# Kernel optimization log

Measured on AMD Instinct MI355X. Metric: run time of the kernel, lower is better.

## Reference

```python
import jax, jax.numpy as jnp
import numpy as np

N, T1, T2 = 150000, 30000, 8192
E1, E2 = 400000, 160000
F_IN, F_HID, F_OUT = 512, 256, 20


def setup_inputs() -> dict:
    key = jax.random.key(0)
    ks = jax.random.split(key, 10)
    return {
        "x": jax.random.normal(ks[0], (N, F_IN), dtype=jnp.float32),
        "src1": jax.random.randint(ks[1], (E1,), 0, N, dtype=jnp.int32),
        "dst1": jax.random.randint(ks[2], (E1,), 0, T1, dtype=jnp.int32),
        "src2": jax.random.randint(ks[3], (E2,), 0, T1, dtype=jnp.int32),
        "dst2": jax.random.randint(ks[4], (E2,), 0, T2, dtype=jnp.int32),
        "Wl1": jax.random.normal(ks[5], (F_HID, F_IN), dtype=jnp.float32) * 0.05,
        "bl1": jnp.zeros((F_HID,), dtype=jnp.float32),
        "Wr1": jax.random.normal(ks[6], (F_HID, F_IN), dtype=jnp.float32) * 0.05,
        "Wl2": jax.random.normal(ks[7], (F_OUT, F_HID), dtype=jnp.float32) * 0.05,
        "bl2": jnp.zeros((F_OUT,), dtype=jnp.float32),
        "Wr2": jax.random.normal(ks[8], (F_OUT, F_HID), dtype=jnp.float32) * 0.05,
    }


def _sage_conv(x_src, x_tgt, src, dst, num_tgt, Wl, bl, Wr):
    # PyG SAGEConv (mean aggr, root_weight=True, bias on lin_l):
    # out = lin_l(mean_{j in N(i)} x_src[j]) + lin_r(x_tgt[i])
    msg = x_src[src]                                                  # [E, F]
    agg = jax.ops.segment_sum(msg, dst, num_segments=num_tgt)        # [T, F]
    cnt = jax.ops.segment_sum(jnp.ones((src.shape[0],), x_src.dtype), dst,
                              num_segments=num_tgt)                  # [T]
    mean = agg / jnp.maximum(cnt, 1.0)[:, None]
    return mean @ Wl.T + bl + x_tgt @ Wr.T


def reference(x, src1, dst1, src2, dst2, Wl1, bl1, Wr1, Wl2, bl2, Wr2):
    # Layer 1: [N, F_IN] -> [T1, F_HID], relu (eval mode: no dropout)
    h = _sage_conv(x, x[:T1], src1, dst1, T1, Wl1, bl1, Wr1)
    h = jax.nn.relu(h)
    # Layer 2: [T1, F_HID] -> [T2, F_OUT]
    out = _sage_conv(h, h[:T2], src2, dst2, T2, Wl2, bl2, Wr2)
    return jax.nn.log_softmax(out, axis=-1)
```

## Files before the change

### kernel.cpp

```cpp
#include <hip/hip_runtime.h>
#include <math.h>

constexpr int T1N  = 30000;
constexpr int T2N  = 8192;
constexpr int FIN  = 512;
constexpr int FHID = 256;
constexpr int FOUT = 20;

typedef short bf16x8 __attribute__((ext_vector_type(8)));
typedef float f32x4  __attribute__((ext_vector_type(4)));

__device__ __forceinline__ short f2bf(float f) {
    unsigned u = __float_as_uint(f);
    u += 0x7fff + ((u >> 16) & 1);
    return (short)(u >> 16);
}

__device__ __forceinline__ void gload16(const void* g, void* l) {
    __builtin_amdgcn_global_load_lds(
        (const __attribute__((address_space(1))) void*)g,
        (__attribute__((address_space(3))) void*)l, 16, 0, 0);
}

__global__ void count_kernel(const int* __restrict__ dst, int* __restrict__ cnt, int E) {
    int i = blockIdx.x * blockDim.x + threadIdx.x;
    int stride = gridDim.x * blockDim.x;
    for (; i < E; i += stride) atomicAdd(&cnt[dst[i]], 1);
}

__global__ __launch_bounds__(1024) void scan_kernel(const int* __restrict__ cnt,
        int* __restrict__ rs, int* __restrict__ cur, int T) {
    __shared__ int wsum[16];
    int tid = threadIdx.x;
    int lane = tid & 63, wid = tid >> 6;
    int carry = 0;
    for (int base = 0; base < T; base += 1024) {
        int i = base + tid;
        int v = (i < T) ? cnt[i] : 0;
        int s = v;
        #pragma unroll
        for (int off = 1; off < 64; off <<= 1) {
            int t = __shfl_up(s, off, 64);
            if (lane >= off) s += t;
        }
        if (lane == 63) wsum[wid] = s;
        __syncthreads();
        if (wid == 0) {
            int w = (lane < 16) ? wsum[lane] : 0;
            #pragma unroll
            for (int off = 1; off < 16; off <<= 1) {
                int t = __shfl_up(w, off, 64);
                if (lane >= off) w += t;
            }
            if (lane < 16) wsum[lane] = w;
        }
        __syncthreads();
        int excl = s - v + (wid > 0 ? wsum[wid - 1] : 0) + carry;
        if (i < T) { rs[i] = excl; cur[i] = excl; }
        int total = wsum[15];
        __syncthreads();
        carry += total;
    }
    if (tid == 0) rs[T] = carry;
}

__global__ void scatter_kernel(const int* __restrict__ src, const int* __restrict__ dst,
        int* __restrict__ cur, int* __restrict__ ss, int E) {
    int i = blockIdx.x * blockDim.x + threadIdx.x;
    int stride = gridDim.x * blockDim.x;
    for (; i < E; i += stride) {
        int d = dst[i];
        int pos = atomicAdd(&cur[d], 1);
        ss[pos] = src[i];
    }
}

__global__ void convert_x_kernel(const float* __restrict__ x, short* __restrict__ A) {
    size_t i = ((size_t)blockIdx.x * blockDim.x + threadIdx.x) * 8;
    if (i >= (size_t)T1N * FIN) return;
    int r = (int)(i >> 9);
    int k = (int)(i & 511);
    const float* p = x + (size_t)r * FIN + k;
    float4 v0 = *(const float4*)p;
    float4 v1 = *(const float4*)(p + 4);
    bf16x8 o;
    o[0] = f2bf(v0.x); o[1] = f2bf(v0.y); o[2] = f2bf(v0.z); o[3] = f2bf(v0.w);
    o[4] = f2bf(v1.x); o[5] = f2bf(v1.y); o[6] = f2bf(v1.z); o[7] = f2bf(v1.w);
    *(bf16x8*)(A + (size_t)r * 1024 + 512 + k) = o;
}

__global__ void convert_w_kernel(const float* __restrict__ Wl, const float* __restrict__ Wr,
        short* __restrict__ Wcat) {
    int i = (blockIdx.x * blockDim.x + threadIdx.x) * 8;
    if (i >= FHID * 1024) return;
    int n = i >> 10;
    int k = i & 1023;
    const float* sp = (k < 512) ? (Wl + (size_t)n * FIN + k) : (Wr + (size_t)n * FIN + (k - 512));
    float4 v0 = *(const float4*)sp;
    float4 v1 = *(const float4*)(sp + 4);
    bf16x8 o;
    o[0] = f2bf(v0.x); o[1] = f2bf(v0.y); o[2] = f2bf(v0.z); o[3] = f2bf(v0.w);
    o[4] = f2bf(v1.x); o[5] = f2bf(v1.y); o[6] = f2bf(v1.z); o[7] = f2bf(v1.w);
    *(bf16x8*)(Wcat + (size_t)n * 1024 + k) = o;
}

template <int F, typename OT, int OSTR>
__global__ void aggregate_kernel(const float* __restrict__ feat, const int* __restrict__ ss,
        const int* __restrict__ rs, OT* __restrict__ mean, int T) {
    int gw = (int)((blockIdx.x * (size_t)blockDim.x + threadIdx.x) >> 6);
    int lane = threadIdx.x & 63;
    if (gw >= T) return;
    int j0 = rs[gw], j1 = rs[gw + 1];
    float4 a0 = make_float4(0.f, 0.f, 0.f, 0.f);
    float4 a1 = make_float4(0.f, 0.f, 0.f, 0.f);
    constexpr int PER = F / 64;
    for (int j = j0; j < j1; ++j) {
        int s = ss[j];
        const float* p = feat + (size_t)s * F + lane * PER;
        float4 v0 = *(const float4*)p;
        a0.x += v0.x; a0.y += v0.y; a0.z += v0.z; a0.w += v0.w;
        if (PER == 8) {
            float4 v1 = *(const float4*)(p + 4);
            a1.x += v1.x; a1.y += v1.y; a1.z += v1.z; a1.w += v1.w;
        }
    }
    int d = j1 - j0;
    float inv = 1.0f / (float)(d > 1 ? d : 1);
    if constexpr (sizeof(OT) == 2) {
        bf16x8 o;
        o[0] = f2bf(a0.x * inv); o[1] = f2bf(a0.y * inv);
        o[2] = f2bf(a0.z * inv); o[3] = f2bf(a0.w * inv);
        o[4] = f2bf(a1.x * inv); o[5] = f2bf(a1.y * inv);
        o[6] = f2bf(a1.z * inv); o[7] = f2bf(a1.w * inv);
        *(bf16x8*)(mean + (size_t)gw * OSTR + lane * PER) = o;
    } else {
        float* o = (float*)(mean + (size_t)gw * OSTR + lane * PER);
        *(float4*)o = make_float4(a0.x * inv, a0.y * inv, a0.z * inv, a0.w * inv);
        if (PER == 8)
            *(float4*)(o + 4) = make_float4(a1.x * inv, a1.y * inv, a1.z * inv, a1.w * inv);
    }
}

__global__ __launch_bounds__(256, 2) void gemm1_mfma(
        const short* __restrict__ A, const short* __restrict__ W,
        const float* __restrict__ bias, float* __restrict__ h) {
    __shared__ short As[128 * 32];
    __shared__ short Bs[128 * 32];
    int tid = threadIdx.x;
    int wid = tid >> 6, lane = tid & 63;
    int brow = blockIdx.x * 128, bcol = blockIdx.y * 128;
    int wr = (wid >> 1) * 64, wc = (wid & 1) * 64;

    f32x4 acc[4][4] = {};

    int kgrp = lane >> 4;
    int r16 = lane & 15;

    for (int kt = 0; kt < 1024; kt += 32) {
        #pragma unroll
        for (int c2 = 0; c2 < 2; ++c2) {
            int q = wid + c2 * 4;
            int c = q * 64 + lane;
            int row = c >> 2;
            int sl = (c & 3) ^ (row & 3);
            int gr = brow + row; if (gr > T1N - 1) gr = T1N - 1;
            gload16(A + (size_t)gr * 1024 + kt + sl * 8, (char*)As + q * 1024);
            gload16(W + (size_t)(bcol + row) * 1024 + kt + sl * 8, (char*)Bs + q * 1024);
        }
        __syncthreads();

        bf16x8 af[4], bfr[4];
        #pragma unroll
        for (int m = 0; m < 4; ++m) {
            int row = wr + m * 16 + r16;
            int sl = kgrp ^ (row & 3);
            af[m] = *(const bf16x8*)((const char*)As + row * 64 + sl * 16);
        }
        #pragma unroll
        for (int n = 0; n < 4; ++n) {
            int row = wc + n * 16 + r16;
            int sl = kgrp ^ (row & 3);
            bfr[n] = *(const bf16x8*)((const char*)Bs + row * 64 + sl * 16);
        }
        #pragma unroll
        for (int m = 0; m < 4; ++m)
            #pragma unroll
            for (int n = 0; n < 4; ++n)
                acc[m][n] = __builtin_amdgcn_mfma_f32_16x16x32_bf16(
                        af[m], bfr[n], acc[m][n], 0, 0, 0);
        __syncthreads();
    }

    int g4 = lane >> 4;
    #pragma unroll
    for (int n = 0; n < 4; ++n) {
        int col = bcol + wc + n * 16 + r16;
        float bv = bias[col];
        #pragma unroll
        for (int m = 0; m < 4; ++m) {
            #pragma unroll
            for (int r = 0; r < 4; ++r) {
                int row = brow + wr + m * 16 + g4 * 4 + r;
                if (row < T1N) {
                    float v = acc[m][n][r] + bv;
                    h[(size_t)row * FHID + col] = v > 0.f ? v : 0.f;
                }
            }
        }
    }
}

__global__ __launch_bounds__(256) void gemm2_lsm_kernel(const float* __restrict__ mean2,
        const float* __restrict__ h, const float* __restrict__ Wl,
        const float* __restrict__ Wr, const float* __restrict__ bias,
        float* __restrict__ out) {
    __shared__ float Wls[FOUT * FHID];
    __shared__ float Wrs[FOUT * FHID];
    int tid = threadIdx.x;
    for (int i = tid; i < FOUT * FHID / 4; i += 256) {
        ((float4*)Wls)[i] = ((const float4*)Wl)[i];
        ((float4*)Wrs)[i] = ((const float4*)Wr)[i];
    }
    __syncthreads();

    int row = blockIdx.x * 4 + (tid >> 6);
    int lane = tid & 63;
    if (row >= T2N) return;

    float acc[FOUT];
    #pragma unroll
    for (int o = 0; o < FOUT; ++o) acc[o] = 0.f;

    const float* mrow = mean2 + (size_t)row * FHID;
    const float* hrow = h + (size_t)row * FHID;
    #pragma unroll
    for (int kk = 0; kk < 4; ++kk) {
        int k = lane + kk * 64;
        float m = mrow[k];
        float hr = hrow[k];
        #pragma unroll
        for (int o = 0; o < FOUT; ++o)
            acc[o] = fmaf(m, Wls[o * FHID + k], fmaf(hr, Wrs[o * FHID + k], acc[o]));
    }
    #pragma unroll
    for (int o = 0; o < FOUT; ++o)
        #pragma unroll
        for (int off = 32; off > 0; off >>= 1)
            acc[o] += __shfl_down(acc[o], off, 64);

    if (lane == 0) {
        float mx = -1e30f;
        #pragma unroll
        for (int o = 0; o < FOUT; ++o) {
            acc[o] += bias[o];
            mx = fmaxf(mx, acc[o]);
        }
        float s = 0.f;
        #pragma unroll
        for (int o = 0; o < FOUT; ++o) s += expf(acc[o] - mx);
        float lse = mx + logf(s);
        float* op = out + (size_t)row * FOUT;
        #pragma unroll
        for (int o = 0; o < FOUT; ++o) op[o] = acc[o] - lse;
    }
}

extern "C" void kernel_launch(void* const* d_in, const int* in_sizes, int n_in,
                              void* d_out, int out_size, void* d_ws, size_t ws_size,
                              hipStream_t stream) {
    const float* x   = (const float*)d_in[0];
    const int* src1  = (const int*)d_in[1];
    const int* dst1  = (const int*)d_in[2];
    const int* src2  = (const int*)d_in[3];
    const int* dst2  = (const int*)d_in[4];
    const float* Wl1 = (const float*)d_in[5];
    const float* bl1 = (const float*)d_in[6];
    const float* Wr1 = (const float*)d_in[7];
    const float* Wl2 = (const float*)d_in[8];
    const float* bl2 = (const float*)d_in[9];
    const float* Wr2 = (const float*)d_in[10];
    int E1 = in_sizes[1];
    int E2 = in_sizes[3];

    char* p = (char*)d_ws;
    auto alloc = [&](size_t bytes) {
        char* r = p;
        p += (bytes + 255) & ~(size_t)255;
        return r;
    };
    short* Abuf  = (short*)alloc((size_t)T1N * 1024 * 2);
    short* Wcat  = (short*)alloc((size_t)FHID * 1024 * 2);
    float* hbuf  = (float*)alloc((size_t)T1N * FHID * 4);
    float* mean2 = (float*)alloc((size_t)T2N * FHID * 4);
    int* cnt1 = (int*)alloc((size_t)T1N * 4);
    int* rs1  = (int*)alloc((size_t)(T1N + 1) * 4);
    int* cur1 = (int*)alloc((size_t)T1N * 4);
    int* ss1  = (int*)alloc((size_t)E1 * 4);
    int* cnt2 = (int*)alloc((size_t)T2N * 4);
    int* rs2  = (int*)alloc((size_t)(T2N + 1) * 4);
    int* cur2 = (int*)alloc((size_t)T2N * 4);
    int* ss2  = (int*)alloc((size_t)E2 * 4);

    hipMemsetAsync(cnt1, 0, (size_t)T1N * 4, stream);
    hipMemsetAsync(cnt2, 0, (size_t)T2N * 4, stream);

    count_kernel<<<512, 256, 0, stream>>>(dst1, cnt1, E1);
    count_kernel<<<256, 256, 0, stream>>>(dst2, cnt2, E2);
    scan_kernel<<<1, 1024, 0, stream>>>(cnt1, rs1, cur1, T1N);
    scan_kernel<<<1, 1024, 0, stream>>>(cnt2, rs2, cur2, T2N);
    scatter_kernel<<<512, 256, 0, stream>>>(src1, dst1, cur1, ss1, E1);
    scatter_kernel<<<256, 256, 0, stream>>>(src2, dst2, cur2, ss2, E2);

    convert_w_kernel<<<(FHID * 1024 / 8 + 255) / 256, 256, 0, stream>>>(Wl1, Wr1, Wcat);
    convert_x_kernel<<<(int)(((size_t)T1N * FIN / 8 + 255) / 256), 256, 0, stream>>>(x, Abuf);

    aggregate_kernel<FIN, short, 1024>
        <<<(T1N * 64 + 255) / 256, 256, 0, stream>>>(x, ss1, rs1, Abuf, T1N);
    dim3 g1((T1N + 127) / 128, FHID / 128);
    gemm1_mfma<<<g1, 256, 0, stream>>>(Abuf, Wcat, bl1, hbuf);

    aggregate_kernel<FHID, float, FHID>
        <<<(T2N * 64 + 255) / 256, 256, 0, stream>>>(hbuf, ss2, rs2, mean2, T2N);
    gemm2_lsm_kernel<<<T2N / 4, 256, 0, stream>>>(mean2, hbuf, Wl2, Wr2, bl2, (float*)d_out);
}
```

Before: 686.4 us.

## Gather bf16 copy of x in aggregation, double-buffer gemm1, vectorize scan

All of x is now converted to bf16 up front, and the layer-1 neighbour gather reads bf16 rows, halving the bytes per random gather at the cost of a full-size conversion pass. The concatenated A buffer is split into separate mean and root buffers that gemm1 reads directly. gemm1 gets double-buffered LDS staging with a revised XOR swizzle to overlap loads with MFMA work. The prefix scan processes four counters per thread with int4 loads and stores, and the two count memsets are merged into one.

```diff
diff --git a/kernel.cpp b/kernel.cpp
--- a/kernel.cpp
+++ b/kernel.cpp
@@ -14,6 +14,9 @@
     unsigned u = __float_as_uint(f);
     u += 0x7fff + ((u >> 16) & 1);
     return (short)(u >> 16);
+}
+__device__ __forceinline__ float bf2f(short s) {
+    return __uint_as_float(((unsigned)(unsigned short)s) << 16);
 }
 
 __device__ __forceinline__ void gload16(const void* g, void* l) {
@@ -34,10 +37,18 @@
     int tid = threadIdx.x;
     int lane = tid & 63, wid = tid >> 6;
     int carry = 0;
-    for (int base = 0; base < T; base += 1024) {
-        int i = base + tid;
-        int v = (i < T) ? cnt[i] : 0;
-        int s = v;
+    for (int base = 0; base < T; base += 4096) {
+        int i = base + tid * 4;
+        int4 v = make_int4(0, 0, 0, 0);
+        if (i + 3 < T) v = *(const int4*)(cnt + i);
+        else {
+            if (i     < T) v.x = cnt[i];
+            if (i + 1 < T) v.y = cnt[i + 1];
+            if (i + 2 < T) v.z = cnt[i + 2];
+            if (i + 3 < T) v.w = cnt[i + 3];
+        }
+        int tsum = v.x + v.y + v.z + v.w;
+        int s = tsum;
         #pragma unroll
         for (int off = 1; off < 64; off <<= 1) {
             int t = __shfl_up(s, off, 64);
@@ -55,8 +66,16 @@
             if (lane < 16) wsum[lane] = w;
         }
         __syncthreads();
-        int excl = s - v + (wid > 0 ? wsum[wid - 1] : 0) + carry;
-        if (i < T) { rs[i] = excl; cur[i] = excl; }
+        int e0 = s - tsum + (wid > 0 ? wsum[wid - 1] : 0) + carry;
+        int e1 = e0 + v.x, e2 = e1 + v.y, e3 = e2 + v.z;
+        if (i + 3 < T) {
+            *(int4*)(rs + i)  = make_int4(e0, e1, e2, e3);
+            *(int4*)(cur + i) = make_int4(e0, e1, e2, e3);
+        } else {
+            if (i     < T) { rs[i]     = e0; cur[i]     = e0; }
+            if (i + 1 < T) { rs[i + 1] = e1; cur[i + 1] = e1; }
+            if (i + 2 < T) { rs[i + 2] = e2; cur[i + 2] = e2; }
+        }
         int total = wsum[15];
         __syncthreads();
         carry += total;
@@ -75,18 +94,16 @@
     }
 }
 
-__global__ void convert_x_kernel(const float* __restrict__ x, short* __restrict__ A) {
-    size_t i = ((size_t)blockIdx.x * blockDim.x + threadIdx.x) * 8;
-    if (i >= (size_t)T1N * FIN) return;
-    int r = (int)(i >> 9);
-    int k = (int)(i & 511);
-    const float* p = x + (size_t)r * FIN + k;
+__global__ void convert_x_full(const float* __restrict__ x, short* __restrict__ xbf, long n8) {
+    long i = ((long)blockIdx.x * blockDim.x + threadIdx.x);
+    if (i >= n8) return;
+    const float* p = x + i * 8;
     float4 v0 = *(const float4*)p;
     float4 v1 = *(const float4*)(p + 4);
     bf16x8 o;
     o[0] = f2bf(v0.x); o[1] = f2bf(v0.y); o[2] = f2bf(v0.z); o[3] = f2bf(v0.w);
     o[4] = f2bf(v1.x); o[5] = f2bf(v1.y); o[6] = f2bf(v1.z); o[7] = f2bf(v1.w);
-    *(bf16x8*)(A + (size_t)r * 1024 + 512 + k) = o;
+    *(bf16x8*)(xbf + i * 8) = o;
 }
 
 __global__ void convert_w_kernel(const float* __restrict__ Wl, const float* __restrict__ Wr,
@@ -104,83 +121,95 @@
     *(bf16x8*)(Wcat + (size_t)n * 1024 + k) = o;
 }
 
-template <int F, typename OT, int OSTR>
-__global__ void aggregate_kernel(const float* __restrict__ feat, const int* __restrict__ ss,
-        const int* __restrict__ rs, OT* __restrict__ mean, int T) {
+__global__ void agg1_kernel(const short* __restrict__ xbf, const int* __restrict__ ss,
+        const int* __restrict__ rs, short* __restrict__ meanbf, int T) {
     int gw = (int)((blockIdx.x * (size_t)blockDim.x + threadIdx.x) >> 6);
     int lane = threadIdx.x & 63;
     if (gw >= T) return;
     int j0 = rs[gw], j1 = rs[gw + 1];
-    float4 a0 = make_float4(0.f, 0.f, 0.f, 0.f);
-    float4 a1 = make_float4(0.f, 0.f, 0.f, 0.f);
-    constexpr int PER = F / 64;
+    float a[8] = {};
     for (int j = j0; j < j1; ++j) {
         int s = ss[j];
-        const float* p = feat + (size_t)s * F + lane * PER;
-        float4 v0 = *(const float4*)p;
-        a0.x += v0.x; a0.y += v0.y; a0.z += v0.z; a0.w += v0.w;
-        if (PER == 8) {
-            float4 v1 = *(const float4*)(p + 4);
-            a1.x += v1.x; a1.y += v1.y; a1.z += v1.z; a1.w += v1.w;
-        }
+        bf16x8 v = *(const bf16x8*)(xbf + (size_t)s * FIN + lane * 8);
+        #pragma unroll
+        for (int q = 0; q < 8; ++q) a[q] += bf2f(v[q]);
     }
     int d = j1 - j0;
     float inv = 1.0f / (float)(d > 1 ? d : 1);
-    if constexpr (sizeof(OT) == 2) {
-        bf16x8 o;
-        o[0] = f2bf(a0.x * inv); o[1] = f2bf(a0.y * inv);
-        o[2] = f2bf(a0.z * inv); o[3] = f2bf(a0.w * inv);
-        o[4] = f2bf(a1.x * inv); o[5] = f2bf(a1.y * inv);
-        o[6] = f2bf(a1.z * inv); o[7] = f2bf(a1.w * inv);
-        *(bf16x8*)(mean + (size_t)gw * OSTR + lane * PER) = o;
-    } else {
-        float* o = (float*)(mean + (size_t)gw * OSTR + lane * PER);
-        *(float4*)o = make_float4(a0.x * inv, a0.y * inv, a0.z * inv, a0.w * inv);
-        if (PER == 8)
-            *(float4*)(o + 4) = make_float4(a1.x * inv, a1.y * inv, a1.z * inv, a1.w * inv);
-    }
+    bf16x8 o;
+    #pragma unroll
+    for (int q = 0; q < 8; ++q) o[q] = f2bf(a[q] * inv);
+    *(bf16x8*)(meanbf + (size_t)gw * FIN + lane * 8) = o;
+}
+
+__global__ void agg2_kernel(const float* __restrict__ feat, const int* __restrict__ ss,
+        const int* __restrict__ rs, float* __restrict__ mean, int T) {
+    int gw = (int)((blockIdx.x * (size_t)blockDim.x + threadIdx.x) >> 6);
+    int lane = threadIdx.x & 63;
+    if (gw >= T) return;
+    int j0 = rs[gw], j1 = rs[gw + 1];
+    float4 a = make_float4(0.f, 0.f, 0.f, 0.f);
+    for (int j = j0; j < j1; ++j) {
+        int s = ss[j];
+        float4 v = *(const float4*)(feat + (size_t)s * FHID + lane * 4);
+        a.x += v.x; a.y += v.y; a.z += v.z; a.w += v.w;
+    }
+    int d = j1 - j0;
+    float inv = 1.0f / (float)(d > 1 ? d : 1);
+    *(float4*)(mean + (size_t)gw * FHID + lane * 4) =
+        make_float4(a.x * inv, a.y * inv, a.z * inv, a.w * inv);
 }
 
 __global__ __launch_bounds__(256, 2) void gemm1_mfma(
-        const short* __restrict__ A, const short* __restrict__ W,
-        const float* __restrict__ bias, float* __restrict__ h) {
-    __shared__ short As[128 * 32];
-    __shared__ short Bs[128 * 32];
+        const short* __restrict__ Am, const short* __restrict__ Ax,
+        const short* __restrict__ W, const float* __restrict__ bias,
+        float* __restrict__ h) {
+    __shared__ short As[2][128 * 32];
+    __shared__ short Bs[2][128 * 32];
     int tid = threadIdx.x;
     int wid = tid >> 6, lane = tid & 63;
     int brow = blockIdx.x * 128, bcol = blockIdx.y * 128;
     int wr = (wid >> 1) * 64, wc = (wid & 1) * 64;
 
     f32x4 acc[4][4] = {};
-
     int kgrp = lane >> 4;
     int r16 = lane & 15;
 
-    for (int kt = 0; kt < 1024; kt += 32) {
+    auto stage = [&](int buf, int kt) {
+        const short* Abase = (kt < 512) ? Am : Ax;
+        int ko = kt & 511;
         #pragma unroll
         for (int c2 = 0; c2 < 2; ++c2) {
             int q = wid + c2 * 4;
             int c = q * 64 + lane;
             int row = c >> 2;
-            int sl = (c & 3) ^ (row & 3);
+            int rx = (row ^ (row >> 2)) & 3;
+            int sl = (c & 3) ^ rx;
             int gr = brow + row; if (gr > T1N - 1) gr = T1N - 1;
-            gload16(A + (size_t)gr * 1024 + kt + sl * 8, (char*)As + q * 1024);
-            gload16(W + (size_t)(bcol + row) * 1024 + kt + sl * 8, (char*)Bs + q * 1024);
-        }
-        __syncthreads();
+            gload16(Abase + (size_t)gr * 512 + ko + sl * 8, (char*)As[buf] + q * 1024);
+            gload16(W + (size_t)(bcol + row) * 1024 + kt + sl * 8, (char*)Bs[buf] + q * 1024);
+        }
+    };
+
+    stage(0, 0);
+    __syncthreads();
+
+    int cur = 0;
+    for (int kt = 0; kt < 1024; kt += 32) {
+        if (kt + 32 < 1024) stage(cur ^ 1, kt + 32);
 
         bf16x8 af[4], bfr[4];
         #pragma unroll
         for (int m = 0; m < 4; ++m) {
             int row = wr + m * 16 + r16;
-            int sl = kgrp ^ (row & 3);
-            af[m] = *(const bf16x8*)((const char*)As + row * 64 + sl * 16);
+            int sl = kgrp ^ ((row ^ (row >> 2)) & 3);
+            af[m] = *(const bf16x8*)((const char*)As[cur] + row * 64 + sl * 16);
         }
         #pragma unroll
         for (int n = 0; n < 4; ++n) {
             int row = wc + n * 16 + r16;
-            int sl = kgrp ^ (row & 3);
-            bfr[n] = *(const bf16x8*)((const char*)Bs + row * 64 + sl * 16);
+            int sl = kgrp ^ ((row ^ (row >> 2)) & 3);
+            bfr[n] = *(const bf16x8*)((const char*)Bs[cur] + row * 64 + sl * 16);
         }
         #pragma unroll
         for (int m = 0; m < 4; ++m)
@@ -188,7 +217,9 @@
             for (int n = 0; n < 4; ++n)
                 acc[m][n] = __builtin_amdgcn_mfma_f32_16x16x32_bf16(
                         af[m], bfr[n], acc[m][n], 0, 0, 0);
+
         __syncthreads();
+        cur ^= 1;
     }
 
     int g4 = lane >> 4;
@@ -281,6 +312,7 @@
     const float* Wr2 = (const float*)d_in[10];
     int E1 = in_sizes[1];
     int E2 = in_sizes[3];
+    int N  = in_sizes[0] / FIN;
 
     char* p = (char*)d_ws;
     auto alloc = [&](size_t bytes) {
@@ -288,21 +320,21 @@
         p += (bytes + 255) & ~(size_t)255;
         return r;
     };
-    short* Abuf  = (short*)alloc((size_t)T1N * 1024 * 2);
+    short* xbf   = (short*)alloc((size_t)N * FIN * 2);
+    short* meanbf= (short*)alloc((size_t)T1N * FIN * 2);
     short* Wcat  = (short*)alloc((size_t)FHID * 1024 * 2);
     float* hbuf  = (float*)alloc((size_t)T1N * FHID * 4);
     float* mean2 = (float*)alloc((size_t)T2N * FHID * 4);
     int* cnt1 = (int*)alloc((size_t)T1N * 4);
+    int* cnt2 = (int*)alloc((size_t)T2N * 4);
     int* rs1  = (int*)alloc((size_t)(T1N + 1) * 4);
     int* cur1 = (int*)alloc((size_t)T1N * 4);
     int* ss1  = (int*)alloc((size_t)E1 * 4);
-    int* cnt2 = (int*)alloc((size_t)T2N * 4);
     int* rs2  = (int*)alloc((size_t)(T2N + 1) * 4);
     int* cur2 = (int*)alloc((size_t)T2N * 4);
     int* ss2  = (int*)alloc((size_t)E2 * 4);
 
-    hipMemsetAsync(cnt1, 0, (size_t)T1N * 4, stream);
-    hipMemsetAsync(cnt2, 0, (size_t)T2N * 4, stream);
+    hipMemsetAsync(cnt1, 0, (size_t)((char*)(cnt2 + T2N) - (char*)cnt1), stream);
 
     count_kernel<<<512, 256, 0, stream>>>(dst1, cnt1, E1);
     count_kernel<<<256, 256, 0, stream>>>(dst2, cnt2, E2);
@@ -312,14 +344,13 @@
     scatter_kernel<<<256, 256, 0, stream>>>(src2, dst2, cur2, ss2, E2);
 
     convert_w_kernel<<<(FHID * 1024 / 8 + 255) / 256, 256, 0, stream>>>(Wl1, Wr1, Wcat);
-    convert_x_kernel<<<(int)(((size_t)T1N * FIN / 8 + 255) / 256), 256, 0, stream>>>(x, Abuf);
-
-    aggregate_kernel<FIN, short, 1024>
-        <<<(T1N * 64 + 255) / 256, 256, 0, stream>>>(x, ss1, rs1, Abuf, T1N);
+    long n8 = (long)N * FIN / 8;
+    convert_x_full<<<(int)((n8 + 255) / 256), 256, 0, stream>>>(x, xbf, n8);
+
+    agg1_kernel<<<(T1N * 64 + 255) / 256, 256, 0, stream>>>(xbf, ss1, rs1, meanbf, T1N);
     dim3 g1((T1N + 127) / 128, FHID / 128);
-    gemm1_mfma<<<g1, 256, 0, stream>>>(Abuf, Wcat, bl1, hbuf);
-
-    aggregate_kernel<FHID, float, FHID>
-        <<<(T2N * 64 + 255) / 256, 256, 0, stream>>>(hbuf, ss2, rs2, mean2, T2N);
+    gemm1_mfma<<<g1, 256, 0, stream>>>(meanbf, xbf, Wcat, bl1, hbuf);
+
+    agg2_kernel<<<(T2N * 64 + 255) / 256, 256, 0, stream>>>(hbuf, ss2, rs2, mean2, T2N);
     gemm2_lsm_kernel<<<T2N / 4, 256, 0, stream>>>(mean2, hbuf, Wl2, Wr2, bl2, (float*)d_out);
 }
```

Result: no change. 685.2 us (-0.2%).
